# Kernel optimization log

Measured on AMD Instinct MI355X. Metric: run time of the kernel, lower is better.

## Reference

```python
import jax, jax.numpy as jnp
import numpy as np

BLOCK_SIZE = 32
BLOCK_COUNTS = 8
N_MAX = 1024  # max seq len across jagged batch (static)
LN_EPS = 1e-5


def _silu(x):
    return x * jax.nn.sigmoid(x)


def setup_inputs() -> dict:
    key = jax.random.key(0)
    ks = jax.random.split(key, 5)
    T, H, D = 3200, 8, 128
    lengths = np.array([1024, 768, 896, 512], dtype=np.int64)
    offsets = np.concatenate([[0], np.cumsum(lengths)]).astype(np.int64)  # [B+1]
    q = jax.random.normal(ks[0], (T, H, D), jnp.float32)
    k = jax.random.normal(ks[1], (T, H, D), jnp.float32)
    v = jax.random.normal(ks[2], (T, H, D), jnp.float32)
    u = jax.random.normal(ks[3], (T, H, D), jnp.float32)
    Wg = jax.random.normal(ks[4], (H, D, 3), jnp.float32) * 0.05
    bg = jnp.zeros((H, 3), jnp.float32)
    return {"q": q, "k": k, "v": v, "u": u, "Wg": Wg, "bg": bg,
            "x_offsets": jnp.asarray(offsets)}


def _to_padded(jag, offsets, lengths, n):
    # jag: [T, H, D] -> [B, n, H, D], zero padded
    pos = jnp.arange(n)
    idx = offsets[:-1, None] + pos[None, :]                # [B, n]
    valid = pos[None, :] < lengths[:, None]                # [B, n]
    g = jag[jnp.clip(idx, 0, jag.shape[0] - 1)]            # [B, n, H, D]
    return jnp.where(valid[..., None, None], g, 0.0)


def _to_jagged(padded, offsets, T):
    tok = jnp.arange(T)
    b = jnp.searchsorted(offsets, tok, side='right') - 1   # batch id per token
    m = tok - offsets[b]                                   # local position
    return padded[b, m]


def _forward(q, k, v, u, Wg, bg, x_offsets):
    T, H, D = q.shape
    B = x_offsets.shape[0] - 1
    n = N_MAX
    bs = BLOCK_SIZE
    nb = n // bs
    S = min(BLOCK_COUNTS, nb)
    scale = D ** (-0.5)
    lengths = x_offsets[1:] - x_offsets[:-1]

    qp = _to_padded(q, x_offsets, lengths, n)  # [B, n, H, D]
    kp = _to_padded(k, x_offsets, lengths, n)
    vp = _to_padded(v, x_offsets, lengths, n)

    # gate model: per-head linear D->3 + sigmoid
    gates = jax.nn.sigmoid(jnp.einsum('bmhd,hde->bmhe', qp, Wg) + bg)
    g_cmp, g_slc = gates[..., 0], gates[..., 1]  # [B, n, H]

    # --- block compression ---
    k_cmp = kp.reshape(B, nb, bs, H, D).mean(axis=2)  # [B, nb, H, D]
    v_cmp = vp.reshape(B, nb, bs, H, D).mean(axis=2)

    # --- compressed attention + top-k block selection ---
    scores = jnp.einsum('bmhd,bkhd->bhmk', qp, k_cmp) * scale  # [B, H, n, nb]
    qblk = jnp.arange(n) // bs
    causal = qblk[:, None] >= jnp.arange(nb)[None, :]          # [n, nb]
    masked_scores = jnp.where(causal[None, None], scores, -jnp.inf)
    _, topk = jax.lax.top_k(masked_scores, S)                  # [B, H, n, S]
    topk = jnp.where(topk > qblk[None, None, :, None], -1, topk)

    p_cmp = jnp.where(causal[None, None], _silu(scores), 0.0)
    o_cmp = jnp.einsum('bhmk,bkhd->bmhd', p_cmp, v_cmp) * g_cmp[..., None]

    # --- selected (gathered top-k block) attention ---
    topk_p = jnp.transpose(topk, (0, 2, 1, 3))                 # [B, n, H, S]
    Kb = kp.reshape(B, nb, bs, H, D).transpose(0, 1, 3, 2, 4)  # [B, nb, H, bs, D]
    Vb = vp.reshape(B, nb, bs, H, D).transpose(0, 1, 3, 2, 4)
    b_ix = jnp.arange(B)[:, None, None]
    h_ix = jnp.arange(H)[None, None, :]
    m_pos = jnp.arange(n)
    off = jnp.arange(bs)

    def body(acc, s_idx):
        blk = jnp.take(topk_p, s_idx, axis=3)                  # [B, n, H]
        blk_c = jnp.maximum(blk, 0)
        Ks = Kb[b_ix, blk_c, h_ix]                             # [B, n, H, bs, D]
        Vs = Vb[b_ix, blk_c, h_ix]
        sc = jnp.einsum('bmhd,bmhkd->bmhk', qp, Ks) * scale    # [B, n, H, bs]
        kpos = blk_c[..., None] * bs + off                     # [B, n, H, bs]
        ok = (blk >= 0)[..., None] & (kpos <= m_pos[None, :, None, None])
        p = jnp.where(ok, _silu(sc), 0.0)
        acc = acc + jnp.einsum('bmhk,bmhkd->bmhd', p, Vs)
        return acc, None

    acc, _ = jax.lax.scan(jax.checkpoint(body), jnp.zeros_like(qp), jnp.arange(S))
    o_slc = acc * g_slc[..., None]

    # back to jagged, LayerNorm over flattened (H*D), gate by u
    o_cmp_j = _to_jagged(o_cmp, x_offsets, T)
    o_slc_j = _to_jagged(o_slc, x_offsets, T)

    def ln_u(x):
        xf = x.reshape(T, H * D)
        mu = xf.mean(-1, keepdims=True)
        var = ((xf - mu) ** 2).mean(-1, keepdims=True)
        xn = (xf - mu) * jax.lax.rsqrt(var + LN_EPS)
        return xn.reshape(T, H, D) * u

    out = ln_u(o_cmp_j) + ln_u(o_slc_j)
    return out, qp, kp


def reference(q, k, v, u, Wg, bg, x_offsets):
    return _forward(q, k, v, u, Wg, bg, x_offsets)
```

## Files before the change

### kernel.cpp

```cpp
#include <hip/hip_runtime.h>
#include <hip/hip_bf16.h>
#include <cmath>

#define H 8
#define D 128
#define HD 1024
#define NMAX 1024
#define BS 32
#define NB 32
#define S_SEL 8
#define CHUNK 8
#define MC 4
#define KP 136
#define NXCD 8
#define SCALE 0.08838834764831845f
#define SENT -3.0e38f

typedef __attribute__((ext_vector_type(8))) short short8;
typedef __attribute__((ext_vector_type(4))) float f32x4;

#define MFMA16(a, b, c) __builtin_amdgcn_mfma_f32_16x16x32_bf16(a, b, c, 0, 0, 0)

__device__ __forceinline__ float silu(float x) {
    return x * __builtin_amdgcn_rcpf(1.f + __expf(-x));
}
__device__ __forceinline__ float sigmoid_fast(float x) {
    return __builtin_amdgcn_rcpf(1.f + __expf(-x));
}
__device__ __forceinline__ unsigned short f2bf(float x) {
    return __builtin_bit_cast(unsigned short, __float2bfloat16(x));
}
__device__ __forceinline__ float bfup(unsigned short b) {
    unsigned u = (unsigned)b << 16;
    return __builtin_bit_cast(float, u);
}
__device__ __forceinline__ void split3(float x, unsigned short& b0,
                                       unsigned short& b1, unsigned short& b2) {
    b0 = f2bf(x);
    float r1 = x - bfup(b0);
    b1 = f2bf(r1);
    float r2 = r1 - bfup(b1);
    b2 = f2bf(r2);
}

__global__ __launch_bounds__(256) void prep_kernel(
    const float* __restrict__ q, const float* __restrict__ k,
    const float* __restrict__ v, const float* __restrict__ Wg,
    const float* __restrict__ bg, const int* __restrict__ offs,
    unsigned short* __restrict__ kb16, unsigned short* __restrict__ vt_blk,
    float* __restrict__ g, unsigned short* __restrict__ kc0,
    unsigned short* __restrict__ kc1, unsigned short* __restrict__ kc2,
    unsigned short* __restrict__ vt_cmp, float* __restrict__ o_slc,
    float* __restrict__ qp, float* __restrict__ kp) {
    int x = blockIdx.x;
    int nt = x & (NB - 1);
    int h = (x >> 5) & 7;
    int b = x >> 8;
    int o0 = offs[b];
    int len = offs[b + 1] - o0;
    int tid = threadIdx.x;
    size_t bh = (size_t)(b * H + h);
    int j = tid >> 3, dc = tid & 7;
    size_t pbase = (size_t)((b * NMAX + nt * BS + j)) * HD + h * D + dc * 16;
    if (nt * BS >= len) {
        if (tid < 128) {
            kc0[(bh * NB + nt) * 128 + tid] = 0;
            kc1[(bh * NB + nt) * 128 + tid] = 0;
            kc2[(bh * NB + nt) * 128 + tid] = 0;
            vt_cmp[(bh * 128 + tid) * NB + nt] = 0;
        }
        if (qp) {
            float4 z = make_float4(0.f, 0.f, 0.f, 0.f);
#pragma unroll
            for (int i = 0; i < 4; i++) {
                *(float4*)(qp + pbase + i * 4) = z;
                *(float4*)(kp + pbase + i * 4) = z;
            }
        }
        return;
    }

    __shared__ __align__(16) unsigned short tile[128 * 40];
    __shared__ float redK[4][128];
    __shared__ float redV[4][128];
    int w = tid >> 6, lane = tid & 63;
    size_t base = (size_t)(o0 + nt * BS + j) * HD + h * D + dc * 16;

    {
        float4 z = make_float4(0.f, 0.f, 0.f, 0.f);
#pragma unroll
        for (int i = 0; i < 4; i++) *(float4*)(o_slc + base + i * 4) = z;
    }

    {
        float xv[16];
        *(float4*)(xv + 0)  = *(const float4*)(k + base);
        *(float4*)(xv + 4)  = *(const float4*)(k + base + 4);
        *(float4*)(xv + 8)  = *(const float4*)(k + base + 8);
        *(float4*)(xv + 12) = *(const float4*)(k + base + 12);
        short8 lo, hi;
#pragma unroll
        for (int i = 0; i < 8; i++) { lo[i] = (short)f2bf(xv[i]); hi[i] = (short)f2bf(xv[8 + i]); }
        *(short8*)(kb16 + base) = lo;
        *(short8*)(kb16 + base + 8) = hi;
        if (kp) {
#pragma unroll
            for (int i = 0; i < 4; i++) *(float4*)(kp + pbase + i * 4) = *(float4*)(xv + i * 4);
        }
#pragma unroll
        for (int i = 0; i < 16; i++) {
            float s = xv[i];
            s += __shfl_xor(s, 8); s += __shfl_xor(s, 16); s += __shfl_xor(s, 32);
            if (lane < 8) redK[w][lane * 16 + i] = s;
        }
    }
    {
        float xv[16];
        *(float4*)(xv + 0)  = *(const float4*)(v + base);
        *(float4*)(xv + 4)  = *(const float4*)(v + base + 4);
        *(float4*)(xv + 8)  = *(const float4*)(v + base + 8);
        *(float4*)(xv + 12) = *(const float4*)(v + base + 12);
#pragma unroll
        for (int i = 0; i < 16; i++) tile[(dc * 16 + i) * 40 + j] = f2bf(xv[i]);
#pragma unroll
        for (int i = 0; i < 16; i++) {
            float s = xv[i];
            s += __shfl_xor(s, 8); s += __shfl_xor(s, 16); s += __shfl_xor(s, 32);
            if (lane < 8) redV[w][lane * 16 + i] = s;
        }
    }
    {
        float xv[16];
        *(float4*)(xv + 0)  = *(const float4*)(q + base);
        *(float4*)(xv + 4)  = *(const float4*)(q + base + 4);
        *(float4*)(xv + 8)  = *(const float4*)(q + base + 8);
        *(float4*)(xv + 12) = *(const float4*)(q + base + 12);
        if (qp) {
#pragma unroll
            for (int i = 0; i < 4; i++) *(float4*)(qp + pbase + i * 4) = *(float4*)(xv + i * 4);
        }
        float p0 = 0.f, p1 = 0.f;
#pragma unroll
        for (int i = 0; i < 16; i++) {
            int wb = (h * D + dc * 16 + i) * 3;
            p0 += xv[i] * Wg[wb + 0];
            p1 += xv[i] * Wg[wb + 1];
        }
#pragma unroll
        for (int off = 4; off > 0; off >>= 1) {
            p0 += __shfl_xor(p0, off);
            p1 += __shfl_xor(p1, off);
        }
        if (dc == 0) {
            float g0 = sigmoid_fast(p0 + bg[h * 3 + 0]);
            float g1 = sigmoid_fast(p1 + bg[h * 3 + 1]);
            float* gp = g + (size_t)((b * NMAX + nt * BS + j) * H + h) * 2;
            gp[0] = g0; gp[1] = g1;
        }
    }
    __syncthreads();
    {
        int d = tid >> 1, hf = tid & 1;
        short8 a = *(const short8*)(tile + d * 40 + hf * 16);
        short8 c = *(const short8*)(tile + d * 40 + hf * 16 + 8);
        size_t ob = ((bh * NB + nt) * 128 + (size_t)d) * 32 + hf * 16;
        *(short8*)(vt_blk + ob) = a;
        *(short8*)(vt_blk + ob + 8) = c;
    }
    if (tid < 128) {
        int d = tid;
        const float inv = 1.f / 32.f;
        float km = (redK[0][d] + redK[1][d] + redK[2][d] + redK[3][d]) * inv;
        float vm = (redV[0][d] + redV[1][d] + redV[2][d] + redV[3][d]) * inv;
        unsigned short e0, e1, e2;
        split3(km, e0, e1, e2);
        kc0[(bh * NB + nt) * 128 + d] = e0;
        kc1[(bh * NB + nt) * 128 + d] = e1;
        kc2[(bh * NB + nt) * 128 + d] = e2;
        vt_cmp[(bh * 128 + d) * NB + nt] = f2bf(vm);
    }
}

__global__ __launch_bounds__(256) void cmp_attn(
    const float* __restrict__ q, const unsigned short* __restrict__ kc0,
    const unsigned short* __restrict__ kc1, const unsigned short* __restrict__ kc2,
    const unsigned short* __restrict__ vt_cmp, const float* __restrict__ g,
    const int* __restrict__ offs, unsigned* __restrict__ ms_g,
    float* __restrict__ o_cmp_j) {
    int x = blockIdx.x;
    int qblk = (NB - 1) - (x & (NB - 1));
    int h = (x >> 5) & 7;
    int b = x >> 8;
    int o0 = offs[b];
    int len = offs[b + 1] - o0;
    if (qblk * BS >= len) return;
    size_t bh = (size_t)(b * H + h);

    __shared__ __align__(16) unsigned short pool[19456];
    __shared__ float Ss[32 * 33];
    unsigned short* R0 = pool;
    unsigned short* R1 = pool + 4352;
    unsigned short* R2 = pool + 8704;
    unsigned short* R3 = pool + 13056;
    unsigned short* Ps = pool + 18176;

    int tid = threadIdx.x;
    int w = tid >> 6, lane = tid & 63;
    int r = lane & 15, quad = lane >> 4;
    int mt = w >> 1, jt = w & 1;
    int stg_j = tid >> 3, stg_dc = tid & 7;

    if (stg_j <= qblk) {
        size_t src = (bh * NB + stg_j) * 128 + stg_dc * 16;
        int ofs = stg_j * 136 + stg_dc * 16;
        short8 a0 = *(const short8*)(kc0 + src);
        short8 b0 = *(const short8*)(kc0 + src + 8);
        short8 a1 = *(const short8*)(kc1 + src);
        short8 b1 = *(const short8*)(kc1 + src + 8);
        short8 a2 = *(const short8*)(kc2 + src);
        short8 b2 = *(const short8*)(kc2 + src + 8);
        *(short8*)(R0 + ofs) = a0; *(short8*)(R0 + ofs + 8) = b0;
        *(short8*)(R1 + ofs) = a1; *(short8*)(R1 + ofs + 8) = b1;
        *(short8*)(R2 + ofs) = a2; *(short8*)(R2 + ofs + 8) = b2;
    }
    {
        int d = tid >> 1, hf = tid & 1;
        short8 vv = *(const short8*)(vt_cmp + (bh * 128 + d) * NB + hf * 16);
        short8 vw = *(const short8*)(vt_cmp + (bh * 128 + d) * NB + hf * 16 + 8);
        *(short8*)(R3 + d * 40 + hf * 16) = vv;
        *(short8*)(R3 + d * 40 + hf * 16 + 8) = vw;
    }
    __syncthreads();

    f32x4 sv = (f32x4){0.f, 0.f, 0.f, 0.f};
    if (jt == 0 || qblk >= 16) {
        short8 qf0[4], qf1[4], qf2[4];
        const float* qrow = q + (size_t)(o0 + qblk * BS + mt * 16 + r) * HD + h * D;
#pragma unroll
        for (int s = 0; s < 4; s++) {
            const float* p0 = qrow + s * 32 + quad * 8;
            float xv[8];
            *(float4*)(xv) = *(const float4*)p0;
            *(float4*)(xv + 4) = *(const float4*)(p0 + 4);
            short8 f0, f1, f2;
#pragma unroll
            for (int i = 0; i < 8; i++) {
                unsigned short e0, e1, e2;
                split3(xv[i], e0, e1, e2);
                f0[i] = (short)e0; f1[i] = (short)e1; f2[i] = (short)e2;
            }
            qf0[s] = f0; qf1[s] = f1; qf2[s] = f2;
        }
#pragma unroll
        for (int s = 0; s < 4; s++) {
            int ofs = (jt * 16 + r) * 136 + s * 32 + quad * 8;
            short8 k0 = *(const short8*)(R0 + ofs);
            short8 k1 = *(const short8*)(R1 + ofs);
            short8 k2 = *(const short8*)(R2 + ofs);
            sv = MFMA16(qf1[s], k1, sv);
            sv = MFMA16(qf0[s], k2, sv);
            sv = MFMA16(qf2[s], k0, sv);
            sv = MFMA16(qf0[s], k1, sv);
            sv = MFMA16(qf1[s], k0, sv);
            sv = MFMA16(qf0[s], k0, sv);
        }
    }
    int colj = jt * 16 + r;
    bool causal = (colj <= qblk);
#pragma unroll
    for (int i = 0; i < 4; i++) {
        int mrow = mt * 16 + quad * 4 + i;
        float sc = sv[i] * SCALE;
        Ss[mrow * 33 + colj] = causal ? sc : SENT;
        Ps[mrow * 40 + colj] = f2bf(causal ? silu(sc) : 0.f);
    }
    __syncthreads();

    f32x4 accC[2][2];
#pragma unroll
    for (int a = 0; a < 2; a++)
#pragma unroll
        for (int c = 0; c < 2; c++) accC[a][c] = (f32x4){0.f, 0.f, 0.f, 0.f};
    {
        short8 pf0 = *(const short8*)(Ps + r * 40 + quad * 8);
        short8 pf1 = *(const short8*)(Ps + (16 + r) * 40 + quad * 8);
        short8 vf0 = *(const short8*)(R3 + ((2 * w + 0) * 16 + r) * 40 + quad * 8);
        short8 vf1 = *(const short8*)(R3 + ((2 * w + 1) * 16 + r) * 40 + quad * 8);
        accC[0][0] = MFMA16(pf0, vf0, accC[0][0]);
        accC[0][1] = MFMA16(pf0, vf1, accC[0][1]);
        accC[1][0] = MFMA16(pf1, vf0, accC[1][0]);
        accC[1][1] = MFMA16(pf1, vf1, accC[1][1]);
    }
    size_t msbase = (bh << 10) + (size_t)qblk * BS;
    if (qblk < S_SEL) {
        if (tid < BS) ms_g[msbase + tid] = (1u << (qblk + 1)) - 1u;
    } else {
        int h2 = lane >> 5, l32 = lane & 31;
#pragma unroll
        for (int pass = 0; pass < 4; pass++) {
            int row = w * 8 + pass * 2 + h2;
            float val = Ss[row * 33 + l32];
            int cnt = 0;
#pragma unroll
            for (int kk = 1; kk < 32; kk++) {
                int jj = (l32 + kk) & 31;
                float ov = __shfl(val, h2 * 32 + jj);
                if ((ov > val) || (ov == val && jj < l32)) cnt++;
            }
            bool sel = (cnt < S_SEL) && (val > -2.9e38f);
            unsigned long long bal = __ballot(sel);
            unsigned mask = (unsigned)(h2 ? (bal >> 32) : (bal & 0xffffffffULL));
            if (l32 == 0) ms_g[msbase + row] = mask;
        }
    }
#pragma unroll
    for (int mtl = 0; mtl < 2; mtl++) {
#pragma unroll
        for (int i = 0; i < 4; i++) {
            int mrow = mtl * 16 + quad * 4 + i;
            int gm = qblk * BS + mrow;
            float gc = g[(size_t)((b * NMAX + gm) * H + h) * 2];
            float* dst = o_cmp_j + (size_t)(o0 + gm) * HD + h * D;
            dst[(2 * w + 0) * 16 + r] = accC[mtl][0][i] * gc;
            dst[(2 * w + 1) * 16 + r] = accC[mtl][1][i] * gc;
        }
    }
}

__global__ __launch_bounds__(256) void slc_attn(
    const float* __restrict__ q, const unsigned short* __restrict__ kb16,
    const unsigned short* __restrict__ vt_blk, const float* __restrict__ g,
    const int* __restrict__ offs, const unsigned* __restrict__ ms_g,
    float* __restrict__ o_slc_j) {
    int x = blockIdx.x;
    int xcd = x & (NXCD - 1);
    int rest = x >> 3;
    int group = rest >> 6;
    int inner = rest & 63;
    int bh = group * NXCD + xcd;
    int b = bh >> 3, h = bh & 7;
    int chunk = inner & (MC - 1);
    int mtile = 15 - (inner >> 2);
    int o0 = offs[b];
    int len = offs[b + 1] - o0;
    if (mtile * 64 >= len) return;
    int qmax = 2 * mtile + 1;
    int kb0 = chunk * CHUNK;
    if (kb0 > qmax) return;
    int kend = min(qmax, kb0 + CHUNK - 1);

    __shared__ __align__(16) unsigned short pool[2 * 32 * KP + 2 * 5120 + 2560];
    __shared__ unsigned Ms[64];
    unsigned short* Kst0 = pool;
    unsigned short* Kst1 = pool + 32 * KP;
    unsigned short* Vst0 = pool + 2 * 32 * KP;
    unsigned short* Vst1 = pool + 2 * 32 * KP + 5120;
    unsigned short* Ps   = pool + 2 * 32 * KP + 10240;

    int tid = threadIdx.x;
    int w = tid >> 6, lane = tid & 63;
    int r = lane & 15, quad = lane >> 4;
    int stg_j = tid >> 3, stg_dc = tid & 7;

    if (tid < 64)
        Ms[tid] = ms_g[((size_t)bh << 10) + mtile * 64 + tid];

    short8 qs[4];
    {
        const float* qrow = q + (size_t)(o0 + mtile * 64 + w * 16 + r) * HD + h * D;
#pragma unroll
        for (int s = 0; s < 4; s++) {
            const float* p0 = qrow + s * 32 + quad * 8;
            float xv[8];
            *(float4*)(xv) = *(const float4*)p0;
            *(float4*)(xv + 4) = *(const float4*)(p0 + 4);
            short8 f;
#pragma unroll
            for (int i = 0; i < 8; i++) f[i] = (short)f2bf(xv[i]);
            qs[s] = f;
        }
    }
    f32x4 acc[8];
#pragma unroll
    for (int a = 0; a < 8; a++) acc[a] = (f32x4){0.f, 0.f, 0.f, 0.f};

    size_t vtbase = (size_t)(bh * NB) * 4096;
    int vd = tid >> 1, vhf = tid & 1;

    {
        const unsigned short* ks = kb16 + (size_t)(o0 + kb0 * BS + stg_j) * HD + h * D + stg_dc * 16;
        short8 k0 = *(const short8*)ks;
        short8 k1 = *(const short8*)(ks + 8);
        *(short8*)(Kst0 + stg_j * KP + stg_dc * 16) = k0;
        *(short8*)(Kst0 + stg_j * KP + stg_dc * 16 + 8) = k1;
        const unsigned short* vs = vt_blk + vtbase + (size_t)kb0 * 4096 + tid * 16;
        short8 v0 = *(const short8*)vs;
        short8 v1 = *(const short8*)(vs + 8);
        *(short8*)(Vst0 + vd * 40 + vhf * 16) = v0;
        *(short8*)(Vst0 + vd * 40 + vhf * 16 + 8) = v1;
    }
    __syncthreads();

    int c = 0;
    for (int kb = kb0; kb <= kend; kb++) {
        short8 pk0, pk1, pv0, pv1;
        bool pf = (kb < kend);
        if (pf) {
            const unsigned short* ks = kb16 + (size_t)(o0 + (kb + 1) * BS + stg_j) * HD + h * D + stg_dc * 16;
            pk0 = *(const short8*)ks;
            pk1 = *(const short8*)(ks + 8);
            const unsigned short* vs = vt_blk + vtbase + (size_t)(kb + 1) * 4096 + tid * 16;
            pv0 = *(const short8*)vs;
            pv1 = *(const short8*)(vs + 8);
        }
        unsigned short* K = c ? Kst1 : Kst0;
        unsigned short* V = c ? Vst1 : Vst0;
        f32x4 s0 = (f32x4){0.f, 0.f, 0.f, 0.f};
        f32x4 s1 = (f32x4){0.f, 0.f, 0.f, 0.f};
#pragma unroll
        for (int s = 0; s < 4; s++) {
            short8 kf0 = *(const short8*)(K + r * KP + s * 32 + quad * 8);
            short8 kf1 = *(const short8*)(K + (16 + r) * KP + s * 32 + quad * 8);
            s0 = MFMA16(qs[s], kf0, s0);
            s1 = MFMA16(qs[s], kf1, s1);
        }
#pragma unroll
        for (int jf = 0; jf < 2; jf++) {
            f32x4 svv = jf ? s1 : s0;
            int colj = jf * 16 + r;
            int kpos = kb * BS + colj;
#pragma unroll
            for (int i = 0; i < 4; i++) {
                int mrow = w * 16 + quad * 4 + i;
                int mpos = mtile * 64 + mrow;
                float p = (((Ms[mrow] >> kb) & 1u) && (kpos <= mpos))
                          ? silu(svv[i] * SCALE) : 0.f;
                Ps[mrow * 40 + colj] = f2bf(p);
            }
        }
        {
            short8 pf8 = *(const short8*)(Ps + (w * 16 + r) * 40 + quad * 8);
#pragma unroll
            for (int nf = 0; nf < 8; nf++) {
                short8 vf = *(const short8*)(V + (nf * 16 + r) * 40 + quad * 8);
                acc[nf] = MFMA16(pf8, vf, acc[nf]);
            }
        }
        if (pf) {
            unsigned short* Kn = c ? Kst0 : Kst1;
            unsigned short* Vn = c ? Vst0 : Vst1;
            *(short8*)(Kn + stg_j * KP + stg_dc * 16) = pk0;
            *(short8*)(Kn + stg_j * KP + stg_dc * 16 + 8) = pk1;
            *(short8*)(Vn + vd * 40 + vhf * 16) = pv0;
            *(short8*)(Vn + vd * 40 + vhf * 16 + 8) = pv1;
        }
        __syncthreads();
        c ^= 1;
    }

    bool single = (qmax < CHUNK);
#pragma unroll
    for (int i = 0; i < 4; i++) {
        int mrow = w * 16 + quad * 4 + i;
        int gm = mtile * 64 + mrow;
        float gs = g[(size_t)((b * NMAX + gm) * H + h) * 2 + 1];
        float* dst = o_slc_j + (size_t)(o0 + gm) * HD + h * D;
#pragma unroll
        for (int nf = 0; nf < 8; nf++) {
            float v0 = acc[nf][i] * gs;
            if (single) dst[nf * 16 + r] = v0;
            else        atomicAdd(dst + nf * 16 + r, v0);
        }
    }
}

__global__ __launch_bounds__(256) void pad_qk_kernel(
    const float* __restrict__ q, const float* __restrict__ k,
    const int* __restrict__ offs,
    float* __restrict__ qp, float* __restrict__ kp) {
    int idx = blockIdx.x * 256 + threadIdx.x;
    int d4 = idx & 31;
    int h  = (idx >> 5) & 7;
    int m  = (idx >> 8) & (NMAX - 1);
    int b  = idx >> 18;
    int o0 = offs[b];
    int len = offs[b + 1] - o0;
    float4 qv = make_float4(0.f, 0.f, 0.f, 0.f);
    float4 kv = qv;
    if (m < len) {
        size_t src = (size_t)(o0 + m) * HD + h * D + d4 * 4;
        qv = *(const float4*)(q + src);
        kv = *(const float4*)(k + src);
    }
    *(float4*)(qp + (size_t)idx * 4) = qv;
    *(float4*)(kp + (size_t)idx * 4) = kv;
}

__global__ __launch_bounds__(256) void ln_combine_kernel(
    const float* __restrict__ oc, const float* __restrict__ os,
    const float* __restrict__ u, float* __restrict__ out) {
    int t = blockIdx.x, tid = threadIdx.x;
    size_t base = (size_t)t * HD;
    float4 xc = *(const float4*)(oc + base + tid * 4);
    float4 xs = *(const float4*)(os + base + tid * 4);
    float4 uu = *(const float4*)(u + base + tid * 4);
    float s_c = xc.x + xc.y + xc.z + xc.w;
    float q_c = xc.x * xc.x + xc.y * xc.y + xc.z * xc.z + xc.w * xc.w;
    float s_s = xs.x + xs.y + xs.z + xs.w;
    float q_s = xs.x * xs.x + xs.y * xs.y + xs.z * xs.z + xs.w * xs.w;
#pragma unroll
    for (int off = 32; off > 0; off >>= 1) {
        s_c += __shfl_xor(s_c, off); q_c += __shfl_xor(q_c, off);
        s_s += __shfl_xor(s_s, off); q_s += __shfl_xor(q_s, off);
    }
    __shared__ float red[4][4];
    int w = tid >> 6, lane = tid & 63;
    if (lane == 0) {
        red[w][0] = s_c; red[w][1] = q_c; red[w][2] = s_s; red[w][3] = q_s;
    }
    __syncthreads();
    float tsc = red[0][0] + red[1][0] + red[2][0] + red[3][0];
    float tqc = red[0][1] + red[1][1] + red[2][1] + red[3][1];
    float tss = red[0][2] + red[1][2] + red[2][2] + red[3][2];
    float tqs = red[0][3] + red[1][3] + red[2][3] + red[3][3];
    const float inv = 1.f / 1024.f;
    float mc = tsc * inv, vc = tqc * inv - mc * mc;
    float ms = tss * inv, vs = tqs * inv - ms * ms;
    float rc = rsqrtf(vc + 1e-5f), rs = rsqrtf(vs + 1e-5f);
    float4 o;
    o.x = ((xc.x - mc) * rc + (xs.x - ms) * rs) * uu.x;
    o.y = ((xc.y - mc) * rc + (xs.y - ms) * rs) * uu.y;
    o.z = ((xc.z - mc) * rc + (xs.z - ms) * rs) * uu.z;
    o.w = ((xc.w - mc) * rc + (xs.w - ms) * rs) * uu.w;
    *(float4*)(out + base + tid * 4) = o;
}

extern "C" void kernel_launch(void* const* d_in, const int* in_sizes, int n_in,
                              void* d_out, int out_size, void* d_ws, size_t ws_size,
                              hipStream_t stream) {
    const float* q  = (const float*)d_in[0];
    const float* k  = (const float*)d_in[1];
    const float* v  = (const float*)d_in[2];
    const float* u  = (const float*)d_in[3];
    const float* Wg = (const float*)d_in[4];
    const float* bg = (const float*)d_in[5];
    const int* offs = (const int*)d_in[6];

    int B = in_sizes[6] - 1;
    int T = in_sizes[0] / HD;

    float* out = (float*)d_out;
    float* qp  = out + (size_t)T * HD;
    float* kp  = qp + (size_t)B * NMAX * HD;

    float* o_cmp_j = out;

    size_t plane = (size_t)B * H * NB * 128;
    char* w = (char*)d_ws;
    unsigned short* kc0 = (unsigned short*)w;  w += plane * 2;
    unsigned short* kc1 = (unsigned short*)w;  w += plane * 2;
    unsigned short* kc2 = (unsigned short*)w;  w += plane * 2;
    unsigned short* vt_cmp = (unsigned short*)w; w += plane * 2;
    float* g     = (float*)w;            w += (size_t)B * NMAX * H * 2 * 4;
    unsigned* ms_g = (unsigned*)w;       w += (size_t)B * H * NMAX * 4;
    float* o_slc_j = (float*)w;          w += (size_t)T * HD * 4;

    size_t kb16_bytes = (size_t)T * HD * 2;
    size_t vt_bytes   = (size_t)B * H * NB * 128 * 32 * 2;
    size_t used = (size_t)(w - (char*)d_ws);
    bool fused_pad = (used + kb16_bytes + vt_bytes <= ws_size);
    char* scr = fused_pad ? w : (char*)kp;
    unsigned short* kb16  = (unsigned short*)scr;
    unsigned short* vt_blk = (unsigned short*)(scr + kb16_bytes);

    int prepBlocks = B * H * NB;
    int cmpAttnBlocks = B * H * NB;
    int slcBlocks  = B * H * 16 * MC;
    int padBlocks  = (B * NMAX * HD / 4) / 256;

    prep_kernel<<<prepBlocks, 256, 0, stream>>>(q, k, v, Wg, bg, offs, kb16, vt_blk,
                                                g, kc0, kc1, kc2, vt_cmp, o_slc_j,
                                                fused_pad ? qp : nullptr,
                                                fused_pad ? kp : nullptr);
    cmp_attn<<<cmpAttnBlocks, 256, 0, stream>>>(q, kc0, kc1, kc2, vt_cmp, g,
                                                offs, ms_g, o_cmp_j);
    slc_attn<<<slcBlocks, 256, 0, stream>>>(q, kb16, vt_blk, g, offs, ms_g, o_slc_j);
    if (!fused_pad)
        pad_qk_kernel<<<padBlocks, 256, 0, stream>>>(q, k, offs, qp, kp);
    ln_combine_kernel<<<T, 256, 0, stream>>>(o_cmp_j, o_slc_j, u, out);
}
```

Baseline: 199.2 us.

## Process 64 query rows per block in compressed attention with register top-k

```diff
diff --git a/kernel.cpp b/kernel.cpp
--- a/kernel.cpp
+++ b/kernel.cpp
@@ -188,16 +188,16 @@
     const int* __restrict__ offs, unsigned* __restrict__ ms_g,
     float* __restrict__ o_cmp_j) {
     int x = blockIdx.x;
-    int qblk = (NB - 1) - (x & (NB - 1));
-    int h = (x >> 5) & 7;
-    int b = x >> 8;
+    int qtile = 15 - (x & 15);
+    int h = (x >> 4) & 7;
+    int b = x >> 7;
     int o0 = offs[b];
     int len = offs[b + 1] - o0;
-    if (qblk * BS >= len) return;
+    if (qtile * 64 >= len) return;
     size_t bh = (size_t)(b * H + h);
-
-    __shared__ __align__(16) unsigned short pool[19456];
-    __shared__ float Ss[32 * 33];
+    int qmax = 2 * qtile + 1;
+
+    __shared__ __align__(16) unsigned short pool[3 * 4352 + 5120 + 2560];
     unsigned short* R0 = pool;
     unsigned short* R1 = pool + 4352;
     unsigned short* R2 = pool + 8704;
@@ -207,10 +207,10 @@
     int tid = threadIdx.x;
     int w = tid >> 6, lane = tid & 63;
     int r = lane & 15, quad = lane >> 4;
-    int mt = w >> 1, jt = w & 1;
     int stg_j = tid >> 3, stg_dc = tid & 7;
-
-    if (stg_j <= qblk) {
+    size_t msbase = (bh << 10) + (size_t)qtile * 64;
+
+    if (stg_j <= qmax) {
         size_t src = (bh * NB + stg_j) * 128 + stg_dc * 16;
         int ofs = stg_j * 136 + stg_dc * 16;
         short8 a0 = *(const short8*)(kc0 + src);
@@ -232,10 +232,9 @@
     }
     __syncthreads();
 
-    f32x4 sv = (f32x4){0.f, 0.f, 0.f, 0.f};
-    if (jt == 0 || qblk >= 16) {
-        short8 qf0[4], qf1[4], qf2[4];
-        const float* qrow = q + (size_t)(o0 + qblk * BS + mt * 16 + r) * HD + h * D;
+    short8 qf0[4], qf1[4], qf2[4];
+    {
+        const float* qrow = q + (size_t)(o0 + qtile * 64 + w * 16 + r) * HD + h * D;
 #pragma unroll
         for (int s = 0; s < 4; s++) {
             const float* p0 = qrow + s * 32 + quad * 8;
@@ -251,9 +250,12 @@
             }
             qf0[s] = f0; qf1[s] = f1; qf2[s] = f2;
         }
+    }
+    auto qk6 = [&](int krow) {
+        f32x4 sv = (f32x4){0.f, 0.f, 0.f, 0.f};
 #pragma unroll
         for (int s = 0; s < 4; s++) {
-            int ofs = (jt * 16 + r) * 136 + s * 32 + quad * 8;
+            int ofs = krow * 136 + s * 32 + quad * 8;
             short8 k0 = *(const short8*)(R0 + ofs);
             short8 k1 = *(const short8*)(R1 + ofs);
             short8 k2 = *(const short8*)(R2 + ofs);
@@ -264,66 +266,76 @@
             sv = MFMA16(qf1[s], k0, sv);
             sv = MFMA16(qf0[s], k0, sv);
         }
-    }
-    int colj = jt * 16 + r;
-    bool causal = (colj <= qblk);
+        return sv;
+    };
+    f32x4 s0 = qk6(r);
+    f32x4 s1 = (f32x4){0.f, 0.f, 0.f, 0.f};
+    if (qtile >= 8) s1 = qk6(16 + r);
+
+    float v0[4], v1[4];
+#pragma unroll
+    for (int jf = 0; jf < 2; jf++) {
+        f32x4 svv = jf ? s1 : s0;
+        int colj = jf * 16 + r;
+#pragma unroll
+        for (int i = 0; i < 4; i++) {
+            int mrow = w * 16 + quad * 4 + i;
+            int qb = 2 * qtile + (mrow >> 5);
+            bool causal = (colj <= qb);
+            float sc = svv[i] * SCALE;
+            float val = causal ? sc : SENT;
+            if (jf) v1[i] = val; else v0[i] = val;
+            Ps[mrow * 40 + colj] = f2bf(causal ? silu(sc) : 0.f);
+        }
+    }
+    if (qtile < 4) {
+        if (tid < 64)
+            ms_g[msbase + tid] = (1u << (2 * qtile + (tid >> 5) + 1)) - 1u;
+    } else {
+#pragma unroll
+        for (int i = 0; i < 4; i++) {
+            float a = v0[i], bb = v1[i];
+            int cnt0 = (bb > a) ? 1 : 0;
+            int cnt1 = (a >= bb) ? 1 : 0;
+#pragma unroll
+            for (int m = 1; m < 16; m++) {
+                float pa = __shfl_xor(a, m);
+                float pb = __shfl_xor(bb, m);
+                int pc = r ^ m;
+                cnt0 += ((pa > a) || (pa == a && pc < r)) ? 1 : 0;
+                cnt0 += (pb > a) ? 1 : 0;
+                cnt1 += ((pa > bb) || (pa == bb)) ? 1 : 0;
+                cnt1 += ((pb > bb) || (pb == bb && pc < r)) ? 1 : 0;
+            }
+            bool sel0 = (cnt0 < S_SEL) && (a > -2.9e38f);
+            bool sel1 = (cnt1 < S_SEL) && (bb > -2.9e38f);
+            unsigned long long bal0 = __ballot(sel0);
+            unsigned long long bal1 = __ballot(sel1);
+            unsigned mask = (unsigned)((bal0 >> (16 * quad)) & 0xFFFFull)
+                          | ((unsigned)((bal1 >> (16 * quad)) & 0xFFFFull) << 16);
+            if (r == 0) ms_g[msbase + w * 16 + quad * 4 + i] = mask;
+        }
+    }
+    f32x4 acc[8];
+#pragma unroll
+    for (int a = 0; a < 8; a++) acc[a] = (f32x4){0.f, 0.f, 0.f, 0.f};
+    {
+        short8 pf8 = *(const short8*)(Ps + (w * 16 + r) * 40 + quad * 8);
+#pragma unroll
+        for (int nf = 0; nf < 8; nf++) {
+            short8 vf = *(const short8*)(R3 + (nf * 16 + r) * 40 + quad * 8);
+            acc[nf] = MFMA16(pf8, vf, acc[nf]);
+        }
+    }
 #pragma unroll
     for (int i = 0; i < 4; i++) {
-        int mrow = mt * 16 + quad * 4 + i;
-        float sc = sv[i] * SCALE;
-        Ss[mrow * 33 + colj] = causal ? sc : SENT;
-        Ps[mrow * 40 + colj] = f2bf(causal ? silu(sc) : 0.f);
-    }
-    __syncthreads();
-
-    f32x4 accC[2][2];
-#pragma unroll
-    for (int a = 0; a < 2; a++)
-#pragma unroll
-        for (int c = 0; c < 2; c++) accC[a][c] = (f32x4){0.f, 0.f, 0.f, 0.f};
-    {
-        short8 pf0 = *(const short8*)(Ps + r * 40 + quad * 8);
-        short8 pf1 = *(const short8*)(Ps + (16 + r) * 40 + quad * 8);
-        short8 vf0 = *(const short8*)(R3 + ((2 * w + 0) * 16 + r) * 40 + quad * 8);
-        short8 vf1 = *(const short8*)(R3 + ((2 * w + 1) * 16 + r) * 40 + quad * 8);
-        accC[0][0] = MFMA16(pf0, vf0, accC[0][0]);
-        accC[0][1] = MFMA16(pf0, vf1, accC[0][1]);
-        accC[1][0] = MFMA16(pf1, vf0, accC[1][0]);
-        accC[1][1] = MFMA16(pf1, vf1, accC[1][1]);
-    }
-    size_t msbase = (bh << 10) + (size_t)qblk * BS;
-    if (qblk < S_SEL) {
-        if (tid < BS) ms_g[msbase + tid] = (1u << (qblk + 1)) - 1u;
-    } else {
-        int h2 = lane >> 5, l32 = lane & 31;
-#pragma unroll
-        for (int pass = 0; pass < 4; pass++) {
-            int row = w * 8 + pass * 2 + h2;
-            float val = Ss[row * 33 + l32];
-            int cnt = 0;
-#pragma unroll
-            for (int kk = 1; kk < 32; kk++) {
-                int jj = (l32 + kk) & 31;
-                float ov = __shfl(val, h2 * 32 + jj);
-                if ((ov > val) || (ov == val && jj < l32)) cnt++;
-            }
-            bool sel = (cnt < S_SEL) && (val > -2.9e38f);
-            unsigned long long bal = __ballot(sel);
-            unsigned mask = (unsigned)(h2 ? (bal >> 32) : (bal & 0xffffffffULL));
-            if (l32 == 0) ms_g[msbase + row] = mask;
-        }
-    }
-#pragma unroll
-    for (int mtl = 0; mtl < 2; mtl++) {
-#pragma unroll
-        for (int i = 0; i < 4; i++) {
-            int mrow = mtl * 16 + quad * 4 + i;
-            int gm = qblk * BS + mrow;
-            float gc = g[(size_t)((b * NMAX + gm) * H + h) * 2];
-            float* dst = o_cmp_j + (size_t)(o0 + gm) * HD + h * D;
-            dst[(2 * w + 0) * 16 + r] = accC[mtl][0][i] * gc;
-            dst[(2 * w + 1) * 16 + r] = accC[mtl][1][i] * gc;
-        }
+        int mrow = w * 16 + quad * 4 + i;
+        int gm = qtile * 64 + mrow;
+        float gc = g[(size_t)((b * NMAX + gm) * H + h) * 2];
+        float* dst = o_cmp_j + (size_t)(o0 + gm) * HD + h * D;
+#pragma unroll
+        for (int nf = 0; nf < 8; nf++)
+            dst[nf * 16 + r] = acc[nf][i] * gc;
     }
 }
 
@@ -574,7 +586,7 @@
     unsigned short* vt_blk = (unsigned short*)(scr + kb16_bytes);
 
     int prepBlocks = B * H * NB;
-    int cmpAttnBlocks = B * H * NB;
+    int cmpAttnBlocks = B * H * 16;
     int slcBlocks  = B * H * 16 * MC;
     int padBlocks  = (B * NMAX * HD / 4) / 256;
 
```

New measurement: 187.7 us. 1.06x faster.
